# Performance work log

Hardware: AMD Instinct MI355X
Metric: run time of the kernel (lower is better)

Reference implementation:

```python
import jax, jax.numpy as jnp
import numpy as np

K = 16          # neighbors per node
EPS = 1e-5      # BatchNorm eps
BN_SCALE = 1.0 / np.sqrt(1.0 + EPS)  # eval BN with running mean=0, var=1


def _knn_idx(x, k):
    # x: [B, N, d] -> idx [B, N, k] of k nearest neighbors (self excluded)
    sq = jnp.sum(x * x, axis=-1)                               # [B, N]
    d2 = sq[:, :, None] + sq[:, None, :] - 2.0 * jnp.einsum('bnd,bmd->bnm', x, x)
    n = x.shape[1]
    d2 = jnp.where(jnp.eye(n, dtype=bool)[None], jnp.inf, d2)  # no self loops
    _, idx = jax.lax.top_k(-d2, k)
    return idx


def _edge_conv(x, idx, W, b, g, be):
    # PyG EdgeConv: max_j MLP([x_i, x_j - x_i]); MLP = Linear+BN(eval)+ReLU
    xj = jax.vmap(lambda xb, ib: xb[ib])(x, idx)               # [B, N, k, d]
    xi = x[:, :, None, :]
    m = jnp.concatenate([jnp.broadcast_to(xi, xj.shape), xj - xi], axis=-1)
    h = m @ W + b                                              # [B, N, k, out]
    h = g * (h * BN_SCALE) + be                                # eval BatchNorm
    h = jax.nn.relu(h)
    return jnp.max(h, axis=2)                                  # scatter-max over k


def setup_inputs() -> dict:
    key = jax.random.key(0)
    ks = jax.random.split(key, 16)
    B, N, D, C = 128, 256, 6, 12

    def w(k_, shape, fan_in):
        return (jax.random.normal(k_, shape, jnp.float32) / np.sqrt(fan_in)).astype(jnp.float32)

    inp = {
        'x':   jax.random.normal(ks[0], (B, N, D), jnp.float32),
        'W1':  w(ks[1], (2 * 6, 64), 12),   'b1': jnp.zeros((64,), jnp.float32),
        'g1':  jnp.ones((64,), jnp.float32), 'be1': jnp.zeros((64,), jnp.float32),
        'W2':  w(ks[2], (2 * 64, 128), 128), 'b2': jnp.zeros((128,), jnp.float32),
        'g2':  jnp.ones((128,), jnp.float32), 'be2': jnp.zeros((128,), jnp.float32),
        'W3':  w(ks[3], (2 * 128, 256), 256), 'b3': jnp.zeros((256,), jnp.float32),
        'g3':  jnp.ones((256,), jnp.float32), 'be3': jnp.zeros((256,), jnp.float32),
        'Wf1': w(ks[4], (256, 128), 256),    'bf1': jnp.zeros((128,), jnp.float32),
        'gf':  jnp.ones((128,), jnp.float32), 'bef': jnp.zeros((128,), jnp.float32),
        'Wf2': w(ks[5], (128, C), 128),      'bf2': jnp.zeros((C,), jnp.float32),
    }
    return inp


def reference(x, W1, b1, g1, be1, W2, b2, g2, be2, W3, b3, g3, be3,
              Wf1, bf1, gf, bef, Wf2, bf2):
    h = _edge_conv(x, _knn_idx(x, K), W1, b1, g1, be1)   # [B, N, 64]
    h = _edge_conv(h, _knn_idx(h, K), W2, b2, g2, be2)   # [B, N, 128]
    h = _edge_conv(h, _knn_idx(h, K), W3, b3, g3, be3)   # [B, N, 256]
    p = jnp.max(h, axis=1)                               # global_max_pool [B, 256]
    f = jax.nn.relu(gf * ((p @ Wf1 + bf1) * BN_SCALE) + bef)
    return f @ Wf2 + bf2                                 # [B, num_classes]
```

## Files before the change

### kernel.cpp

```cpp
#include <hip/hip_runtime.h>
#include <cstdint>
#include <cstddef>

#define KNN 16
#define NPTS 256
#define NBATCH 128

static constexpr float BN_SCALE_F = 0.9999950000374997f;

__device__ inline unsigned int f32_ord(float f) {
    unsigned int u = __float_as_uint(f);
    return (u & 0x80000000u) ? ~u : (u | 0x80000000u);
}

__device__ __forceinline__ int wmap(int n) { return n + 4 * (n >> 4); }

template<int D>
__global__ __launch_bounds__(256) void sq_kernel(const float* __restrict__ x,
                                                 float* __restrict__ sq) {
    const int t = blockIdx.x * 256 + threadIdx.x;
    const float* r = x + (size_t)t * D;
    float s = 0.f;
    #pragma unroll
    for (int d = 0; d < D; ++d) s = fmaf(r[d], r[d], s);
    sq[t] = s;
}

template<int D>
__global__ __launch_bounds__(256) void knn_fused_kernel(
        const float* __restrict__ x, const float* __restrict__ sq,
        int* __restrict__ idx) {
    constexpr int KS = (D >= 16) ? 16 : D;
    const int t  = threadIdx.x;
    const int tx = t & 15, ty = t >> 4;
    const int sr = t >> 2, sc = t & 3;
    const int b  = blockIdx.x >> 2;
    const int i0 = (blockIdx.x & 3) * 64;
    const int base = b * NPTS;

    __shared__ float As[KS][68];
    __shared__ float Bs[KS][68];
    __shared__ float d2L[64][65];
    __shared__ unsigned short Mi[64][68];

    unsigned int Lv[16], Li[16];
    #pragma unroll
    for (int q = 0; q < 16; ++q) { Lv[q] = 0xFFFFFFFFu; Li[q] = 0u; }

    for (int jt = 0; jt < 4; ++jt) {
        const int j0 = jt * 64;
        float acc[4][4] = {};
        for (int k0 = 0; k0 < D; k0 += KS) {
            if constexpr (D % 16 == 0) {
                const int r  = t >> 2;
                const int cq = (t & 3) * 4;
                const float4 va = *(const float4*)(x + (size_t)(base + i0 + r) * D + k0 + cq);
                const float4 vb = *(const float4*)(x + (size_t)(base + j0 + r) * D + k0 + cq);
                As[cq + 0][r] = va.x; As[cq + 1][r] = va.y;
                As[cq + 2][r] = va.z; As[cq + 3][r] = va.w;
                Bs[cq + 0][r] = vb.x; Bs[cq + 1][r] = vb.y;
                Bs[cq + 2][r] = vb.z; Bs[cq + 3][r] = vb.w;
            } else {
                for (int e = t; e < 64 * KS; e += 256) {
                    const int r = e / KS, c = e % KS;
                    As[c][r] = x[(size_t)(base + i0 + r) * D + k0 + c];
                    Bs[c][r] = x[(size_t)(base + j0 + r) * D + k0 + c];
                }
            }
            __syncthreads();
            #pragma unroll
            for (int kk = 0; kk < KS; ++kk) {
                const float4 av = *(const float4*)&As[kk][ty * 4];
                const float4 bv = *(const float4*)&Bs[kk][tx * 4];
                const float am[4] = {av.x, av.y, av.z, av.w};
                const float bm[4] = {bv.x, bv.y, bv.z, bv.w};
                #pragma unroll
                for (int m = 0; m < 4; ++m)
                    #pragma unroll
                    for (int n = 0; n < 4; ++n)
                        acc[m][n] = fmaf(am[m], bm[n], acc[m][n]);
            }
            __syncthreads();
        }

        float sqi[4], sqj[4];
        #pragma unroll
        for (int m = 0; m < 4; ++m) {
            sqi[m] = sq[base + i0 + ty * 4 + m];
            sqj[m] = sq[base + j0 + tx * 4 + m];
        }
        #pragma unroll
        for (int m = 0; m < 4; ++m) {
            const int gi = i0 + ty * 4 + m;
            #pragma unroll
            for (int n = 0; n < 4; ++n) {
                float v = (sqi[m] + sqj[n]) - 2.f * acc[m][n];
                if (gi == j0 + tx * 4 + n) v = INFINITY;
                d2L[ty * 4 + m][tx * 4 + n] = v;
            }
        }
        __syncthreads();

        #pragma unroll
        for (int i = 0; i < 16; ++i) {
            const unsigned int v = f32_ord(d2L[sr][sc * 16 + i]);
            const unsigned int j = (unsigned int)(j0 + sc * 16 + i);
            #pragma unroll
            for (int q = 15; q >= 1; --q) {
                const bool a = v < Lv[q];
                const bool c = v < Lv[q - 1];
                Lv[q] = a ? (c ? Lv[q - 1] : v) : Lv[q];
                Li[q] = a ? (c ? Li[q - 1] : j) : Li[q];
            }
            const bool a0 = v < Lv[0];
            Lv[0] = a0 ? v : Lv[0];
            Li[0] = a0 ? j : Li[0];
        }
    }

    __syncthreads();
    #pragma unroll
    for (int q = 0; q < 16; ++q) {
        d2L[sr][sc * 16 + q] = __uint_as_float(Lv[q]);
        Mi[sr][sc * 16 + q]  = (unsigned short)Li[q];
    }
    __syncthreads();

    if (t < 64) {
        const int row = t;
        int h[4];
        unsigned int cv[4], ci[4];
        #pragma unroll
        for (int c = 0; c < 4; ++c) {
            h[c]  = 0;
            cv[c] = __float_as_uint(d2L[row][c * 16]);
            ci[c] = Mi[row][c * 16];
        }
        int outj[16];
        #pragma unroll
        for (int rd = 0; rd < 16; ++rd) {
            unsigned int bv = cv[0], bi = ci[0];
            int bc = 0;
            #pragma unroll
            for (int c = 1; c < 4; ++c) {
                const bool tk = (cv[c] < bv) | ((cv[c] == bv) & (ci[c] < bi));
                bv = tk ? cv[c] : bv;
                bi = tk ? ci[c] : bi;
                bc = tk ? c     : bc;
            }
            outj[rd] = (int)bi;
            #pragma unroll
            for (int c = 0; c < 4; ++c) {
                if (c == bc) {
                    const int hn = h[c] + 1;
                    h[c] = hn;
                    if (hn < 16) {
                        cv[c] = __float_as_uint(d2L[row][c * 16 + hn]);
                        ci[c] = Mi[row][c * 16 + hn];
                    } else {
                        cv[c] = 0xFFFFFFFFu;
                    }
                }
            }
        }
        int4* op = (int4*)(idx + (size_t)(base + i0 + row) * KNN);
        op[0] = make_int4(outj[0],  outj[1],  outj[2],  outj[3]);
        op[1] = make_int4(outj[4],  outj[5],  outj[6],  outj[7]);
        op[2] = make_int4(outj[8],  outj[9],  outj[10], outj[11]);
        op[3] = make_int4(outj[12], outj[13], outj[14], outj[15]);
    }
}

template<int D, int C>
__global__ __launch_bounds__(256) void mlp_gemm_kernel(
        const float* __restrict__ x, const float* __restrict__ W,
        const float* __restrict__ bias, const float* __restrict__ g,
        const float* __restrict__ be,
        float* __restrict__ A, float* __restrict__ Bv) {
    constexpr int BM = 128;
    constexpr int KT = (D >= 16) ? 16 : D;
    const int t  = threadIdx.x;
    const int m0 = blockIdx.x * BM;
    const int n0 = blockIdx.y * 128;
    const int tx = t & 15;
    const int ty = t >> 4;

    __shared__ float Xs[KT][BM + 4];
    __shared__ float Ws[KT][160];

    float acc[8][8] = {};

    for (int k0 = 0; k0 < D; k0 += KT) {
        if constexpr (D % 16 == 0) {
            const int r  = t >> 1;
            const int cq = (t & 1) * 8;
            const float* src = x + (size_t)(m0 + r) * D + k0 + cq;
            const float4 v0 = *(const float4*)(src);
            const float4 v1 = *(const float4*)(src + 4);
            Xs[cq + 0][r] = v0.x; Xs[cq + 1][r] = v0.y;
            Xs[cq + 2][r] = v0.z; Xs[cq + 3][r] = v0.w;
            Xs[cq + 4][r] = v1.x; Xs[cq + 5][r] = v1.y;
            Xs[cq + 6][r] = v1.z; Xs[cq + 7][r] = v1.w;
        } else {
            for (int e = t; e < BM * KT; e += 256) {
                const int r = e / KT, c = e % KT;
                Xs[c][r] = x[(size_t)(m0 + r) * D + k0 + c];
            }
        }
        if constexpr (D % 16 == 0) {
            const int wk = t >> 4;
            const int nq = (t & 15) * 8;
            const int mb = wmap(nq);
            const int gn = n0 + nq;
            const int kr = k0 + wk;
            if (gn < C) {
                const float* pt = W + (size_t)kr * C + gn;
                const float* pb = W + (size_t)(D + kr) * C + gn;
                const float4 t0 = *(const float4*)(pt);
                const float4 t1 = *(const float4*)(pt + 4);
                const float4 b0 = *(const float4*)(pb);
                const float4 b1 = *(const float4*)(pb + 4);
                *(float4*)&Ws[wk][mb]     = make_float4(t0.x - b0.x, t0.y - b0.y,
                                                        t0.z - b0.z, t0.w - b0.w);
                *(float4*)&Ws[wk][mb + 4] = make_float4(t1.x - b1.x, t1.y - b1.y,
                                                        t1.z - b1.z, t1.w - b1.w);
            } else {
                const float* pb = W + (size_t)(D + kr) * C + (gn - C);
                *(float4*)&Ws[wk][mb]     = *(const float4*)(pb);
                *(float4*)&Ws[wk][mb + 4] = *(const float4*)(pb + 4);
            }
        } else {
            for (int e = t; e < KT * 128; e += 256) {
                const int k = e >> 7, n = e & 127;
                const int gn = n0 + n, kr = k0 + k;
                Ws[k][wmap(n)] = (gn < C)
                    ? W[(size_t)kr * C + gn] - W[(size_t)(D + kr) * C + gn]
                    : W[(size_t)(D + kr) * C + (gn - C)];
            }
        }
        __syncthreads();

        const int mc = wmap(tx * 8);
        #pragma unroll
        for (int kk = 0; kk < KT; ++kk) {
            float xm[8], wn[8];
            *(float4*)&xm[0] = *(const float4*)&Xs[kk][ty * 8];
            *(float4*)&xm[4] = *(const float4*)&Xs[kk][ty * 8 + 4];
            *(float4*)&wn[0] = *(const float4*)&Ws[kk][mc];
            *(float4*)&wn[4] = *(const float4*)&Ws[kk][mc + 4];
            #pragma unroll
            for (int m = 0; m < 8; ++m)
                #pragma unroll
                for (int n = 0; n < 8; ++n)
                    acc[m][n] = fmaf(xm[m], wn[n], acc[m][n]);
        }
        __syncthreads();
    }

    const int gn = n0 + tx * 8;
    if (gn < C) {
        float fac[8];
        #pragma unroll
        for (int e = 0; e < 8; ++e) fac[e] = g[gn + e] * BN_SCALE_F;
        #pragma unroll
        for (int m = 0; m < 8; ++m) {
            float o[8];
            #pragma unroll
            for (int e = 0; e < 8; ++e) o[e] = fac[e] * acc[m][e];
            float* dst = A + (size_t)(m0 + ty * 8 + m) * C + gn;
            *(float4*)(dst)     = make_float4(o[0], o[1], o[2], o[3]);
            *(float4*)(dst + 4) = make_float4(o[4], o[5], o[6], o[7]);
        }
    } else {
        const int cb = gn - C;
        float fac[8], bb[8], bee[8];
        #pragma unroll
        for (int e = 0; e < 8; ++e) {
            fac[e] = g[cb + e] * BN_SCALE_F;
            bb[e]  = bias[cb + e];
            bee[e] = be[cb + e];
        }
        #pragma unroll
        for (int m = 0; m < 8; ++m) {
            float o[8];
            #pragma unroll
            for (int e = 0; e < 8; ++e)
                o[e] = fmaf(fac[e], acc[m][e] + bb[e], bee[e]);
            float* dst = Bv + (size_t)(m0 + ty * 8 + m) * C + cb;
            *(float4*)(dst)     = make_float4(o[0], o[1], o[2], o[3]);
            *(float4*)(dst + 4) = make_float4(o[4], o[5], o[6], o[7]);
        }
    }
}

template<int C>
__global__ __launch_bounds__(C) void combine_kernel(
        const float* A, const float* __restrict__ Bv,
        const int* __restrict__ idx, float* out) {
    const int bi = blockIdx.x;
    const int c  = threadIdx.x;
    __shared__ int nbr[KNN];
    if (c < KNN) nbr[c] = idx[(size_t)bi * KNN + c];
    __syncthreads();
    const int b0 = bi & ~255;
    float mx = -INFINITY;
    #pragma unroll
    for (int kk = 0; kk < KNN; ++kk)
        mx = fmaxf(mx, Bv[(size_t)(b0 + nbr[kk]) * C + c]);
    float a = A[(size_t)bi * C + c];
    out[(size_t)bi * C + c] = fmaxf(a + mx, 0.f);
}

__global__ __launch_bounds__(256) void head_kernel(
        const float* __restrict__ h3, const float* __restrict__ Wf1,
        const float* __restrict__ bf1, const float* __restrict__ gf,
        const float* __restrict__ bef, const float* __restrict__ Wf2,
        const float* __restrict__ bf2, float* __restrict__ out) {
    const int b   = blockIdx.x;
    const int tid = threadIdx.x;
    __shared__ float p[256];
    __shared__ float f[128];
    const float* hb = h3 + (size_t)b * NPTS * 256;
    float mx = -INFINITY;
    for (int n = 0; n < NPTS; ++n) mx = fmaxf(mx, hb[(size_t)n * 256 + tid]);
    p[tid] = mx;
    __syncthreads();
    if (tid < 128) {
        float acc = bf1[tid];
        for (int d = 0; d < 256; ++d)
            acc = fmaf(p[d], Wf1[(size_t)d * 128 + tid], acc);
        float v = gf[tid] * (acc * BN_SCALE_F) + bef[tid];
        f[tid] = fmaxf(v, 0.f);
    }
    __syncthreads();
    if (tid < 12) {
        float acc = bf2[tid];
        for (int d = 0; d < 128; ++d)
            acc = fmaf(f[d], Wf2[(size_t)d * 12 + tid], acc);
        out[(size_t)b * 12 + tid] = acc;
    }
}

extern "C" void kernel_launch(void* const* d_in, const int* in_sizes, int n_in,
                              void* d_out, int out_size, void* d_ws, size_t ws_size,
                              hipStream_t stream) {
    const float* x   = (const float*)d_in[0];
    const float* W1  = (const float*)d_in[1];
    const float* b1  = (const float*)d_in[2];
    const float* g1  = (const float*)d_in[3];
    const float* be1 = (const float*)d_in[4];
    const float* W2  = (const float*)d_in[5];
    const float* b2  = (const float*)d_in[6];
    const float* g2  = (const float*)d_in[7];
    const float* be2 = (const float*)d_in[8];
    const float* W3  = (const float*)d_in[9];
    const float* b3  = (const float*)d_in[10];
    const float* g3  = (const float*)d_in[11];
    const float* be3 = (const float*)d_in[12];
    const float* Wf1 = (const float*)d_in[13];
    const float* bf1 = (const float*)d_in[14];
    const float* gf  = (const float*)d_in[15];
    const float* bef = (const float*)d_in[16];
    const float* Wf2 = (const float*)d_in[17];
    const float* bf2 = (const float*)d_in[18];
    float* out = (float*)d_out;

    char* ws = (char*)d_ws;
    const size_t idx_bytes = (size_t)NBATCH * NPTS * KNN * sizeof(int);
    const size_t reg_bytes = (size_t)NBATCH * NPTS * 256 * sizeof(float);
    int*   idx = (int*)ws;
    float* R1  = (float*)(ws + idx_bytes);
    float* R2  = (float*)(ws + idx_bytes + reg_bytes);
    float* R3  = (float*)(ws + idx_bytes + 2 * reg_bytes);
    float* sqb = (float*)(ws + idx_bytes + 3 * reg_bytes);

    const int BN = NBATCH * NPTS;
    const int KNN_GRID = NBATCH * 4;
    const int MB = BN / 128;

    sq_kernel<6><<<BN / 256, 256, 0, stream>>>(x, sqb);
    knn_fused_kernel<6><<<KNN_GRID, 256, 0, stream>>>(x, sqb, idx);
    mlp_gemm_kernel<6, 64><<<dim3(MB, 1), 256, 0, stream>>>(
        x, W1, b1, g1, be1, R1, R2);
    combine_kernel<64><<<BN, 64, 0, stream>>>(R1, R2, idx, R1);

    sq_kernel<64><<<BN / 256, 256, 0, stream>>>(R1, sqb);
    knn_fused_kernel<64><<<KNN_GRID, 256, 0, stream>>>(R1, sqb, idx);
    mlp_gemm_kernel<64, 128><<<dim3(MB, 2), 256, 0, stream>>>(
        R1, W2, b2, g2, be2, R2, R3);
    combine_kernel<128><<<BN, 128, 0, stream>>>(R2, R3, idx, R2);

    sq_kernel<128><<<BN / 256, 256, 0, stream>>>(R2, sqb);
    knn_fused_kernel<128><<<KNN_GRID, 256, 0, stream>>>(R2, sqb, idx);
    mlp_gemm_kernel<128, 256><<<dim3(MB, 4), 256, 0, stream>>>(
        R2, W3, b3, g3, be3, R3, R1);
    combine_kernel<256><<<BN, 256, 0, stream>>>(R3, R1, idx, R3);

    head_kernel<<<NBATCH, 256, 0, stream>>>(R3, Wf1, bf1, gf, bef, Wf2, bf2, out);
}
```

Measured before the change: 470.0 us.

## Retile kNN kernel to 32 query rows per block with 8-way top-k split

The kNN kernel now gives each block 32 query rows against 128-column tiles, doubling the grid to 8 blocks per batch. Each query row's candidate scan is split across 8 threads instead of 4, so each thread's sorted insertion list covers fewer candidates. The final merge is 8-way, done by 32 threads. The intent is more blocks and occupancy (launch bounds 256,4) and shorter serial insertion chains, at the cost of a longer 8-way merge and more redundant loads of the column operand.

```diff
diff --git a/kernel.cpp b/kernel.cpp
--- a/kernel.cpp
+++ b/kernel.cpp
@@ -27,43 +27,52 @@
 }
 
 template<int D>
-__global__ __launch_bounds__(256) void knn_fused_kernel(
+__global__ __launch_bounds__(256, 4) void knn_fused_kernel(
         const float* __restrict__ x, const float* __restrict__ sq,
         int* __restrict__ idx) {
     constexpr int KS = (D >= 16) ? 16 : D;
     const int t  = threadIdx.x;
-    const int tx = t & 15, ty = t >> 4;
-    const int sr = t >> 2, sc = t & 3;
-    const int b  = blockIdx.x >> 2;
-    const int i0 = (blockIdx.x & 3) * 64;
+    const int tx = t & 31, ty = t >> 5;
+    const int sr = t >> 3, sc = t & 7;
+    const int b  = blockIdx.x >> 3;
+    const int i0 = (blockIdx.x & 7) * 32;
     const int base = b * NPTS;
 
-    __shared__ float As[KS][68];
-    __shared__ float Bs[KS][68];
-    __shared__ float d2L[64][65];
-    __shared__ unsigned short Mi[64][68];
+    __shared__ float As[KS][36];
+    __shared__ float Bs[KS][132];
+    __shared__ float d2L[32][132];
+    __shared__ unsigned char Mi[32][128];
 
     unsigned int Lv[16], Li[16];
     #pragma unroll
     for (int q = 0; q < 16; ++q) { Lv[q] = 0xFFFFFFFFu; Li[q] = 0u; }
 
-    for (int jt = 0; jt < 4; ++jt) {
-        const int j0 = jt * 64;
+    for (int jt = 0; jt < 2; ++jt) {
+        const int j0 = jt * 128;
         float acc[4][4] = {};
         for (int k0 = 0; k0 < D; k0 += KS) {
             if constexpr (D % 16 == 0) {
-                const int r  = t >> 2;
-                const int cq = (t & 3) * 4;
-                const float4 va = *(const float4*)(x + (size_t)(base + i0 + r) * D + k0 + cq);
-                const float4 vb = *(const float4*)(x + (size_t)(base + j0 + r) * D + k0 + cq);
-                As[cq + 0][r] = va.x; As[cq + 1][r] = va.y;
-                As[cq + 2][r] = va.z; As[cq + 3][r] = va.w;
-                Bs[cq + 0][r] = vb.x; Bs[cq + 1][r] = vb.y;
-                Bs[cq + 2][r] = vb.z; Bs[cq + 3][r] = vb.w;
+                if (t < 128) {
+                    const int r = t >> 2, cq = (t & 3) * 4;
+                    const float4 va = *(const float4*)(x + (size_t)(base + i0 + r) * D + k0 + cq);
+                    As[cq + 0][r] = va.x; As[cq + 1][r] = va.y;
+                    As[cq + 2][r] = va.z; As[cq + 3][r] = va.w;
+                }
+                #pragma unroll
+                for (int u = 0; u < 2; ++u) {
+                    const int q = t + u * 256;
+                    const int r = q >> 2, cq = (q & 3) * 4;
+                    const float4 vb = *(const float4*)(x + (size_t)(base + j0 + r) * D + k0 + cq);
+                    Bs[cq + 0][r] = vb.x; Bs[cq + 1][r] = vb.y;
+                    Bs[cq + 2][r] = vb.z; Bs[cq + 3][r] = vb.w;
+                }
             } else {
-                for (int e = t; e < 64 * KS; e += 256) {
+                for (int e = t; e < 32 * KS; e += 256) {
                     const int r = e / KS, c = e % KS;
                     As[c][r] = x[(size_t)(base + i0 + r) * D + k0 + c];
+                }
+                for (int e = t; e < 128 * KS; e += 256) {
+                    const int r = e / KS, c = e % KS;
                     Bs[c][r] = x[(size_t)(base + j0 + r) * D + k0 + c];
                 }
             }
@@ -71,9 +80,10 @@
             #pragma unroll
             for (int kk = 0; kk < KS; ++kk) {
                 const float4 av = *(const float4*)&As[kk][ty * 4];
-                const float4 bv = *(const float4*)&Bs[kk][tx * 4];
+                const float2 b0 = *(const float2*)&Bs[kk][tx * 4];
+                const float2 b1 = *(const float2*)&Bs[kk][tx * 4 + 2];
                 const float am[4] = {av.x, av.y, av.z, av.w};
-                const float bm[4] = {bv.x, bv.y, bv.z, bv.w};
+                const float bm[4] = {b0.x, b0.y, b1.x, b1.y};
                 #pragma unroll
                 for (int m = 0; m < 4; ++m)
                     #pragma unroll
@@ -85,10 +95,9 @@
 
         float sqi[4], sqj[4];
         #pragma unroll
-        for (int m = 0; m < 4; ++m) {
-            sqi[m] = sq[base + i0 + ty * 4 + m];
-            sqj[m] = sq[base + j0 + tx * 4 + m];
-        }
+        for (int m = 0; m < 4; ++m) sqi[m] = sq[base + i0 + ty * 4 + m];
+        #pragma unroll
+        for (int n = 0; n < 4; ++n) sqj[n] = sq[base + j0 + tx * 4 + n];
         #pragma unroll
         for (int m = 0; m < 4; ++m) {
             const int gi = i0 + ty * 4 + m;
@@ -103,8 +112,8 @@
 
         #pragma unroll
         for (int i = 0; i < 16; ++i) {
-            const unsigned int v = f32_ord(d2L[sr][sc * 16 + i]);
-            const unsigned int j = (unsigned int)(j0 + sc * 16 + i);
+            const unsigned int v = f32_ord(d2L[sr][sc + 8 * i]);
+            const unsigned int j = (unsigned int)(j0 + sc + 8 * i);
             #pragma unroll
             for (int q = 15; q >= 1; --q) {
                 const bool a = v < Lv[q];
@@ -121,20 +130,20 @@
     __syncthreads();
     #pragma unroll
     for (int q = 0; q < 16; ++q) {
-        d2L[sr][sc * 16 + q] = __uint_as_float(Lv[q]);
-        Mi[sr][sc * 16 + q]  = (unsigned short)Li[q];
+        d2L[sr][sc + 8 * q] = __uint_as_float(Lv[q]);
+        Mi[sr][sc + 8 * q]  = (unsigned char)Li[q];
     }
     __syncthreads();
 
-    if (t < 64) {
+    if (t < 32) {
         const int row = t;
-        int h[4];
-        unsigned int cv[4], ci[4];
-        #pragma unroll
-        for (int c = 0; c < 4; ++c) {
+        int h[8];
+        unsigned int cv[8], ci[8];
+        #pragma unroll
+        for (int c = 0; c < 8; ++c) {
             h[c]  = 0;
-            cv[c] = __float_as_uint(d2L[row][c * 16]);
-            ci[c] = Mi[row][c * 16];
+            cv[c] = __float_as_uint(d2L[row][c]);
+            ci[c] = Mi[row][c];
         }
         int outj[16];
         #pragma unroll
@@ -142,7 +151,7 @@
             unsigned int bv = cv[0], bi = ci[0];
             int bc = 0;
             #pragma unroll
-            for (int c = 1; c < 4; ++c) {
+            for (int c = 1; c < 8; ++c) {
                 const bool tk = (cv[c] < bv) | ((cv[c] == bv) & (ci[c] < bi));
                 bv = tk ? cv[c] : bv;
                 bi = tk ? ci[c] : bi;
@@ -150,13 +159,13 @@
             }
             outj[rd] = (int)bi;
             #pragma unroll
-            for (int c = 0; c < 4; ++c) {
+            for (int c = 0; c < 8; ++c) {
                 if (c == bc) {
                     const int hn = h[c] + 1;
                     h[c] = hn;
                     if (hn < 16) {
-                        cv[c] = __float_as_uint(d2L[row][c * 16 + hn]);
-                        ci[c] = Mi[row][c * 16 + hn];
+                        cv[c] = __float_as_uint(d2L[row][c + 8 * hn]);
+                        ci[c] = Mi[row][c + 8 * hn];
                     } else {
                         cv[c] = 0xFFFFFFFFu;
                     }
@@ -375,7 +384,7 @@
     float* sqb = (float*)(ws + idx_bytes + 3 * reg_bytes);
 
     const int BN = NBATCH * NPTS;
-    const int KNN_GRID = NBATCH * 4;
+    const int KNN_GRID = NBATCH * 8;
     const int MB = BN / 128;
 
     sq_kernel<6><<<BN / 256, 256, 0, stream>>>(x, sqb);
```

Measured after the change: 491.6 us. 1.05x slower.
